# Performance work log

Measured on AMD Instinct MI355X. Metric: run time of the kernel, lower is better.

The kernel has to match this reference:

```python
import jax, jax.numpy as jnp
import numpy as np

N, C, H, W = 4, 256, 64, 64  # in_channels == out_channels == C


def conv1x1(x, w, b):
    # x: [N, Cin, H, W], w: [Cout, Cin], b: [Cout]
    return jnp.einsum('nchw,oc->nohw', x, w) + b[None, :, None, None]


def setup_inputs() -> dict:
    key = jax.random.key(0)
    ks = jax.random.split(key, 4)
    scale = 1.0 / np.sqrt(C)
    return {
        'x': jax.random.normal(ks[0], (N, C, H, W), dtype=jnp.float32),
        'theta_w': jax.random.normal(ks[1], (C, C), dtype=jnp.float32) * scale,
        'theta_b': jnp.zeros((C,), dtype=jnp.float32),
        'phi_w': jax.random.normal(ks[2], (C, C), dtype=jnp.float32) * scale,
        'phi_b': jnp.zeros((C,), dtype=jnp.float32),
        'conv1_w': jax.random.normal(ks[3], (C, C), dtype=jnp.float32) * scale,
        'conv1_b': jnp.zeros((C,), dtype=jnp.float32),
    }


def reference(x, theta_w, theta_b, phi_w, phi_b, conv1_w, conv1_b):
    n, c, h, w = x.shape
    hw = h * w
    theta = conv1x1(x, theta_w, theta_b).reshape(n, c, hw)   # queries [N,C,HW]
    phi = conv1x1(x, phi_w, phi_b).reshape(n, c, hw)         # keys    [N,C,HW]
    g = x.reshape(n, c, hw)                                   # values  [N,C,HW]
    # f = einsum('niab,nicd->nabcd') flattened: [N, HW_q, HW_k]
    scores = jnp.einsum('ncp,ncq->npq', theta, phi) / jnp.sqrt(jnp.asarray(c, x.dtype))
    attn = jax.nn.softmax(scores, axis=-1)                    # softmax over keys
    # f = einsum('nabcd,nicd->niab'): weighted sum of values
    f = jnp.einsum('npq,ncq->ncp', attn, g).reshape(n, c, h, w)
    result = conv1x1(f, conv1_w, conv1_b)
    return x + result
```

## Files before the change

### kernel.cpp

```cpp
#include <hip/hip_runtime.h>
#include <hip/hip_bf16.h>

typedef __attribute__((ext_vector_type(8))) short short8;
typedef __attribute__((ext_vector_type(4))) short short4_t;
typedef __attribute__((ext_vector_type(4))) float float4_t;
typedef unsigned short ushort;

#define HW 4096
#define CC 256
#define NBATCH 4
#define SEQ ((size_t)NBATCH * HW)

static __device__ __forceinline__ unsigned short f2b(float f) {
    union { float f; unsigned u; } v; v.f = f;
    unsigned r = v.u + 0x7FFF + ((v.u >> 16) & 1);
    return (unsigned short)(r >> 16);
}
static __device__ __forceinline__ float b2f(unsigned short u) {
    union { unsigned u; float f; } v; v.u = ((unsigned)u) << 16;
    return v.f;
}

__global__ __launch_bounds__(256) void k_prep(const float* __restrict__ x,
                                              const float* __restrict__ tw,
                                              const float* __restrict__ pw,
                                              const float* __restrict__ cw,
                                              unsigned short* __restrict__ XT,
                                              unsigned short* __restrict__ gb,
                                              unsigned short* __restrict__ Wbt,
                                              unsigned short* __restrict__ Wbp,
                                              unsigned short* __restrict__ Wbc) {
    __shared__ float T[64][65];
    int fb = blockIdx.x + 64 * (blockIdx.y + 4 * blockIdx.z);
    if (fb < 768) {
        int i = fb * 256 + threadIdx.x;
        int sel = i >> 16, off = i & 65535;
        const float* s = sel == 0 ? tw : (sel == 1 ? pw : cw);
        unsigned short* d = sel == 0 ? Wbt : (sel == 1 ? Wbp : Wbc);
        d[off] = f2b(s[off]);
    }
    int n = blockIdx.z, c0 = blockIdx.y * 64, p0 = blockIdx.x * 64;
    int t = threadIdx.x;
    int pl = t & 63, rg = t >> 6;
    const float* xp = x + ((size_t)n * CC + c0) * HW + p0;
    #pragma unroll
    for (int i = 0; i < 16; i++) {
        int cl = rg * 16 + i;
        float v = xp[(size_t)cl * HW + pl];
        T[cl][pl] = v;
        gb[((size_t)n * CC + c0 + cl) * HW + p0 + pl] = f2b(v);
    }
    __syncthreads();
    int cl = t & 63, pg = t >> 6;
    unsigned short* xt = XT + ((size_t)n * HW + p0) * CC + c0;
    #pragma unroll
    for (int i = 0; i < 16; i++) {
        int plw = pg * 16 + i;
        xt[(size_t)plw * CC + cl] = f2b(T[cl][plw]);
    }
}

__global__ __launch_bounds__(256) void k_proj(const unsigned short* __restrict__ XT,
                                              const unsigned short* __restrict__ Wt,
                                              const unsigned short* __restrict__ Wp,
                                              const float* __restrict__ bt,
                                              const float* __restrict__ bp,
                                              unsigned short* __restrict__ outT_t,
                                              unsigned short* __restrict__ outT_p) {
    const unsigned short* W; const float* b; unsigned short* outT;
    if (blockIdx.y == 0) { W = Wt; b = bt; outT = outT_t; }
    else                 { W = Wp; b = bp; outT = outT_p; }
    int w = threadIdx.x >> 6, lane = threadIdx.x & 63;
    int nidx = lane & 15, quad = lane >> 4;
    size_t row0 = (size_t)blockIdx.x * 64 + w * 16;
    float4_t acc[16];
    #pragma unroll
    for (int i = 0; i < 16; i++) acc[i] = (float4_t)(0.f);
    const unsigned short* arow = XT + (row0 + nidx) * CC + quad * 8;
    for (int ks = 0; ks < 8; ks++) {
        short8 a = *(const short8*)(arow + ks * 32);
        #pragma unroll
        for (int cb = 0; cb < 16; cb++) {
            short8 bb = *(const short8*)(W + (size_t)(cb * 16 + nidx) * CC + ks * 32 + quad * 8);
            acc[cb] = __builtin_amdgcn_mfma_f32_16x16x32_bf16(a, bb, acc[cb], 0, 0, 0);
        }
    }
    #pragma unroll
    for (int cb = 0; cb < 16; cb++) {
        int co = cb * 16 + nidx;
        float bias = b[co];
        #pragma unroll
        for (int r = 0; r < 4; r++) {
            size_t prow = row0 + quad * 4 + r;
            outT[prow * CC + co] = f2b(acc[cb][r] + bias);
        }
    }
}

__global__ __launch_bounds__(512)
void k_attn(const unsigned short* __restrict__ thetaT,
            const unsigned short* __restrict__ phiT,
            const unsigned short* __restrict__ gb,
            ushort* __restrict__ Ow, float* __restrict__ lw) {
    __shared__ __align__(16) ushort Kl[2][16384];
    __shared__ __align__(16) ushort Pbuf[2][16][64][8];
    __shared__ float Lbuf[2][128];

    const int tid = threadIdx.x;
    const int w = tid >> 6, lane = tid & 63;
    const int nidx = lane & 15, quad = lane >> 4;
    const int qg = w & 3;
    const int kh = w >> 2;
    const int nb = (blockIdx.x & 7) >> 1;
    const int h  = blockIdx.x & 1;
    const int qtile = blockIdx.x >> 3;
    const int p0 = qtile * 128;
    const size_t seq0 = (size_t)nb * HW;
    const ushort* Kg = phiT + seq0 * CC;
    const ushort* Vg = gb + (size_t)nb * CC * HW;
    const int k00 = h * 2048;

    short8 th[2][8];
    #pragma unroll
    for (int qs = 0; qs < 2; qs++) {
        const ushort* qrow = thetaT + (seq0 + p0 + qg * 32 + qs * 16 + nidx) * CC + quad * 8;
        #pragma unroll
        for (int kb = 0; kb < 8; kb++) th[qs][kb] = *(const short8*)(qrow + kb * 32);
    }

    float4_t o[2][8];
    #pragma unroll
    for (int i = 0; i < 2; i++)
        #pragma unroll
        for (int j = 0; j < 8; j++) o[i][j] = (float4_t)(0.f);
    float lrow[2] = {0.f, 0.f};

    const int c_s = tid >> 4, n_s = tid & 15;
    const int kfbase = (c_s >> 2) * 512 + ((c_s & 3) * 16 + n_s) * 8;
    auto loadKregs = [&](short8 (&kr)[4], int tt) {
        #pragma unroll
        for (int rr = 0; rr < 4; rr++)
            kr[rr] = *(const short8*)(Kg + (size_t)(k00 + tt * 64 + rr * 16 + n_s) * CC + c_s * 8);
    };
    auto stageK = [&](int buf, const short8 (&kr)[4]) {
        #pragma unroll
        for (int rr = 0; rr < 4; rr++) *(short8*)(&Kl[buf][rr * 4096 + kfbase]) = kr[rr];
    };
    auto loadVregs = [&](short8 (&vr)[4], int tt) {
        #pragma unroll
        for (int mg = 0; mg < 2; mg++)
            #pragma unroll
            for (int kst = 0; kst < 2; kst++)
                vr[mg * 2 + kst] = *(const short8*)(Vg + (size_t)(w * 32 + mg * 16 + nidx) * HW
                                                    + k00 + tt * 64 + kst * 32 + quad * 8);
    };

    const float SC = 0.0625f * 1.44269504088896f;
    const int Gp = quad >> 1;
    const int pcell_lo = (nidx ^ (Gp * 4));
    const int pj0 = (quad & 1) * 4;
    const int prcell = ((lane >> 4) << 4) | ((lane & 15) ^ (((lane >> 4) & 1) * 4));

    float4_t s00, s01, s10, s11;
    auto expPhase = [&](int buf) {
        short4_t pk;
        #pragma unroll
        for (int r = 0; r < 4; r++) {
            float e = exp2f(s00[r] * SC); lrow[0] += e; pk[r] = (short)f2b(e);
        }
        *(short4_t*)(&Pbuf[buf][(qg * 2 + 0) * 2 + kh][(0 * 2 + Gp) * 16 + pcell_lo][pj0]) = pk;
        #pragma unroll
        for (int r = 0; r < 4; r++) {
            float e = exp2f(s01[r] * SC); lrow[1] += e; pk[r] = (short)f2b(e);
        }
        *(short4_t*)(&Pbuf[buf][(qg * 2 + 1) * 2 + kh][(0 * 2 + Gp) * 16 + pcell_lo][pj0]) = pk;
        #pragma unroll
        for (int r = 0; r < 4; r++) {
            float e = exp2f(s10[r] * SC); lrow[0] += e; pk[r] = (short)f2b(e);
        }
        *(short4_t*)(&Pbuf[buf][(qg * 2 + 0) * 2 + kh][(1 * 2 + Gp) * 16 + pcell_lo][pj0]) = pk;
        #pragma unroll
        for (int r = 0; r < 4; r++) {
            float e = exp2f(s11[r] * SC); lrow[1] += e; pk[r] = (short)f2b(e);
        }
        *(short4_t*)(&Pbuf[buf][(qg * 2 + 1) * 2 + kh][(1 * 2 + Gp) * 16 + pcell_lo][pj0]) = pk;
    };

    short8 kregs[4], vA[4], vB[4];

    auto ITER = [&](int t, const short8 (&vCur)[4], short8 (&vNext)[4]) {
        const int pb = t & 1;
        const int kbuf = (t + 1) & 1;
        s00 = (float4_t)(0.f); s01 = (float4_t)(0.f);
        s10 = (float4_t)(0.f); s11 = (float4_t)(0.f);
        #pragma unroll
        for (int i = 0; i < 8; i++) {
            short8 k0 = *(const short8*)(&Kl[kbuf][((kh * 2 + 0) * 8 + i) * 512 + lane * 8]);
            short8 k1 = *(const short8*)(&Kl[kbuf][((kh * 2 + 1) * 8 + i) * 512 + lane * 8]);
            s00 = __builtin_amdgcn_mfma_f32_16x16x32_bf16(k0, th[0][i], s00, 0, 0, 0);
            s01 = __builtin_amdgcn_mfma_f32_16x16x32_bf16(k0, th[1][i], s01, 0, 0, 0);
            s10 = __builtin_amdgcn_mfma_f32_16x16x32_bf16(k1, th[0][i], s10, 0, 0, 0);
            s11 = __builtin_amdgcn_mfma_f32_16x16x32_bf16(k1, th[1][i], s11, 0, 0, 0);
            short8 pf0 = *(const short8*)(&Pbuf[pb][i * 2 + 0][prcell][0]);
            short8 pf1 = *(const short8*)(&Pbuf[pb][i * 2 + 1][prcell][0]);
            o[0][i] = __builtin_amdgcn_mfma_f32_16x16x32_bf16(vCur[0], pf0, o[0][i], 0, 0, 0);
            o[0][i] = __builtin_amdgcn_mfma_f32_16x16x32_bf16(vCur[1], pf1, o[0][i], 0, 0, 0);
            o[1][i] = __builtin_amdgcn_mfma_f32_16x16x32_bf16(vCur[2], pf0, o[1][i], 0, 0, 0);
            o[1][i] = __builtin_amdgcn_mfma_f32_16x16x32_bf16(vCur[3], pf1, o[1][i], 0, 0, 0);
        }
        loadVregs(vNext, t + 1);
        expPhase((t + 1) & 1);
        if (t < 30) {
            stageK((t + 2) & 1, kregs);
            loadKregs(kregs, (t + 3 < 32) ? t + 3 : 31);
        }
        __syncthreads();
    };

    loadKregs(kregs, 0); loadVregs(vA, 0);
    stageK(0, kregs);
    loadKregs(kregs, 1);
    __syncthreads();
    s00 = (float4_t)(0.f); s01 = (float4_t)(0.f); s10 = (float4_t)(0.f); s11 = (float4_t)(0.f);
    #pragma unroll
    for (int kb = 0; kb < 8; kb++) {
        short8 k0 = *(const short8*)(&Kl[0][((kh * 2 + 0) * 8 + kb) * 512 + lane * 8]);
        short8 k1 = *(const short8*)(&Kl[0][((kh * 2 + 1) * 8 + kb) * 512 + lane * 8]);
        s00 = __builtin_amdgcn_mfma_f32_16x16x32_bf16(k0, th[0][kb], s00, 0, 0, 0);
        s01 = __builtin_amdgcn_mfma_f32_16x16x32_bf16(k0, th[1][kb], s01, 0, 0, 0);
        s10 = __builtin_amdgcn_mfma_f32_16x16x32_bf16(k1, th[0][kb], s10, 0, 0, 0);
        s11 = __builtin_amdgcn_mfma_f32_16x16x32_bf16(k1, th[1][kb], s11, 0, 0, 0);
    }
    expPhase(0);
    stageK(1, kregs);
    loadKregs(kregs, 2);
    __syncthreads();

    #pragma unroll 1
    for (int tt = 0; tt < 15; tt++) {
        ITER(tt * 2, vA, vB);
        ITER(tt * 2 + 1, vB, vA);
    }
    ITER(30, vA, vB);
    #pragma unroll
    for (int i = 0; i < 8; i++) {
        short8 pf0 = *(const short8*)(&Pbuf[1][i * 2 + 0][prcell][0]);
        short8 pf1 = *(const short8*)(&Pbuf[1][i * 2 + 1][prcell][0]);
        o[0][i] = __builtin_amdgcn_mfma_f32_16x16x32_bf16(vB[0], pf0, o[0][i], 0, 0, 0);
        o[0][i] = __builtin_amdgcn_mfma_f32_16x16x32_bf16(vB[1], pf1, o[0][i], 0, 0, 0);
        o[1][i] = __builtin_amdgcn_mfma_f32_16x16x32_bf16(vB[2], pf0, o[1][i], 0, 0, 0);
        o[1][i] = __builtin_amdgcn_mfma_f32_16x16x32_bf16(vB[3], pf1, o[1][i], 0, 0, 0);
    }

    #pragma unroll
    for (int qs = 0; qs < 2; qs++) {
        float v = lrow[qs];
        v += __shfl_xor(v, 16);
        v += __shfl_xor(v, 32);
        if (quad == 0) Lbuf[kh][qg * 32 + qs * 16 + nidx] = v;
    }
    __syncthreads();
    if (tid < 128)
        lw[(size_t)h * SEQ + seq0 + p0 + tid] = Lbuf[0][tid] + Lbuf[1][tid];
    ushort* Op = Ow + ((size_t)h * SEQ + seq0 + p0) * CC;
    #pragma unroll
    for (int mg = 0; mg < 2; mg++)
        #pragma unroll
        for (int qq = 0; qq < 8; qq++) {
            short4_t pk;
            #pragma unroll
            for (int r = 0; r < 4; r++) pk[r] = (short)f2b(o[mg][qq][r]);
            *(short4_t*)(Op + (size_t)(qq * 16 + nidx) * CC + w * 32 + mg * 16 + quad * 4) = pk;
        }
}

__global__ __launch_bounds__(256) void k_reduce(const ushort* __restrict__ Ow,
                                                const float* __restrict__ lw,
                                                unsigned short* __restrict__ fT) {
    const short8* O0 = (const short8*)Ow;
    const short8* O1 = (const short8*)(Ow + SEQ * CC);
    int i0 = blockIdx.x * 256 + threadIdx.x;
    #pragma unroll
    for (int j = 0; j < 4; j++) {
        int idx = j * 131072 + i0;
        int row = idx >> 5;
        float li = 1.0f / (lw[row] + lw[SEQ + row]);
        short8 a = O0[idx];
        short8 b = O1[idx];
        short8 pk;
        #pragma unroll
        for (int r = 0; r < 8; r++)
            pk[r] = (short)f2b((b2f((ushort)a[r]) + b2f((ushort)b[r])) * li);
        *(short8*)(fT + (size_t)idx * 8) = pk;
    }
}

__global__ __launch_bounds__(256) void k_final(const unsigned short* __restrict__ Wc,
                                               const float* __restrict__ bc,
                                               const unsigned short* __restrict__ fT,
                                               const float* __restrict__ x,
                                               float* __restrict__ out) {
    int w = threadIdx.x >> 6, lane = threadIdx.x & 63;
    int nidx = lane & 15, quad = lane >> 4;
    int n = blockIdx.z;
    int co0 = blockIdx.y * 64 + w * 16;
    int p0 = blockIdx.x * 64;
    float4_t acc[4];
    #pragma unroll
    for (int i = 0; i < 4; i++) acc[i] = (float4_t)(0.f);
    const unsigned short* arow = Wc + (size_t)(co0 + nidx) * CC + quad * 8;
    const unsigned short* brow = fT + ((size_t)n * HW + p0 + nidx) * CC + quad * 8;
    for (int ks = 0; ks < 8; ks++) {
        short8 a = *(const short8*)(arow + ks * 32);
        #pragma unroll
        for (int pb = 0; pb < 4; pb++) {
            short8 bb = *(const short8*)(brow + (size_t)pb * 16 * CC + ks * 32);
            acc[pb] = __builtin_amdgcn_mfma_f32_16x16x32_bf16(a, bb, acc[pb], 0, 0, 0);
        }
    }
    #pragma unroll
    for (int pb = 0; pb < 4; pb++) {
        #pragma unroll
        for (int r = 0; r < 4; r++) {
            int co = co0 + quad * 4 + r;
            size_t idx = ((size_t)n * CC + co) * HW + p0 + pb * 16 + nidx;
            out[idx] = x[idx] + bc[co] + acc[pb][r];
        }
    }
}

extern "C" void kernel_launch(void* const* d_in, const int* in_sizes, int n_in,
                              void* d_out, int out_size, void* d_ws, size_t ws_size,
                              hipStream_t stream) {
    const float* x       = (const float*)d_in[0];
    const float* theta_w = (const float*)d_in[1];
    const float* theta_b = (const float*)d_in[2];
    const float* phi_w   = (const float*)d_in[3];
    const float* phi_b   = (const float*)d_in[4];
    const float* conv1_w = (const float*)d_in[5];
    const float* conv1_b = (const float*)d_in[6];
    float* out = (float*)d_out;

    unsigned short* XT  = (unsigned short*)d_ws;
    unsigned short* gb  = XT  + SEQ * CC;
    unsigned short* thT = gb  + SEQ * CC;
    unsigned short* phT = thT + SEQ * CC;
    unsigned short* fT  = phT + SEQ * CC;
    unsigned short* Wbt = fT  + SEQ * CC;
    unsigned short* Wbp = Wbt + 65536;
    unsigned short* Wbc = Wbp + 65536;
    unsigned short* Ow  = Wbc + 65536;
    float* lw = (float*)(Ow + 2 * SEQ * CC);

    k_prep<<<dim3(64, 4, 4), 256, 0, stream>>>(x, theta_w, phi_w, conv1_w, XT, gb, Wbt, Wbp, Wbc);
    k_proj<<<dim3(256, 2), 256, 0, stream>>>(XT, Wbt, Wbp, theta_b, phi_b, thT, phT);
    k_attn<<<dim3(256), 512, 0, stream>>>(thT, phT, gb, Ow, lw);
    k_reduce<<<dim3(512), 256, 0, stream>>>(Ow, lw, fT);
    k_final<<<dim3(64, 4, 4), 256, 0, stream>>>(Wbc, conv1_b, fT, x, out);
}
```

Baseline: 213.4 us.

## Restructure attention kernel into smaller blocks with direct global-to-LDS K staging

The attention kernel now uses 256-thread blocks covering 64 queries each, with 512 blocks instead of 256. It uses a 32-key tile and 64 iterations, and each wave splits the channel dimension of V instead of the key dimension. K tiles are staged with global_load_lds (direct global-to-LDS), which removes the register round-trip and the K prefetch registers. The goal is more resident blocks, lower register and LDS pressure, and fewer staging instructions. The cost is twice as many loop iterations and barriers, and each block re-reads K and V for fewer queries, which doubles global K/V traffic.

Measured after the change: 322.0 us. +50.9%, slower.

```diff
diff --git a/kernel.cpp b/kernel.cpp
--- a/kernel.cpp
+++ b/kernel.cpp
@@ -10,6 +10,12 @@
 #define CC 256
 #define NBATCH 4
 #define SEQ ((size_t)NBATCH * HW)
+#define KT 32
+#define NT 64
+
+#define GLDS(g, l) __builtin_amdgcn_global_load_lds( \
+    (const __attribute__((address_space(1))) void*)(g), \
+    (__attribute__((address_space(3))) void*)(l), 16, 0, 0)
 
 static __device__ __forceinline__ unsigned short f2b(float f) {
     union { float f; unsigned u; } v; v.f = f;
@@ -97,24 +103,24 @@
     }
 }
 
-__global__ __launch_bounds__(512)
+__global__ __launch_bounds__(256)
 void k_attn(const unsigned short* __restrict__ thetaT,
             const unsigned short* __restrict__ phiT,
             const unsigned short* __restrict__ gb,
             ushort* __restrict__ Ow, float* __restrict__ lw) {
-    __shared__ __align__(16) ushort Kl[2][16384];
-    __shared__ __align__(16) ushort Pbuf[2][16][64][8];
-    __shared__ float Lbuf[2][128];
+    __shared__ __align__(16) ushort Kl[2][8192];
+    __shared__ __align__(16) ushort Pbuf[2][4][64][8];
+    __shared__ float Lbuf[2][64];
 
     const int tid = threadIdx.x;
     const int w = tid >> 6, lane = tid & 63;
     const int nidx = lane & 15, quad = lane >> 4;
-    const int qg = w & 3;
-    const int kh = w >> 2;
+    const int qg = w >> 1;
+    const int sub = w & 1;
     const int nb = (blockIdx.x & 7) >> 1;
     const int h  = blockIdx.x & 1;
     const int qtile = blockIdx.x >> 3;
-    const int p0 = qtile * 128;
+    const int p0 = qtile * 64;
     const size_t seq0 = (size_t)nb * HW;
     const ushort* Kg = phiT + seq0 * CC;
     const ushort* Vg = gb + (size_t)nb * CC * HW;
@@ -128,128 +134,91 @@
         for (int kb = 0; kb < 8; kb++) th[qs][kb] = *(const short8*)(qrow + kb * 32);
     }
 
-    float4_t o[2][8];
-    #pragma unroll
-    for (int i = 0; i < 2; i++)
-        #pragma unroll
-        for (int j = 0; j < 8; j++) o[i][j] = (float4_t)(0.f);
+    float4_t o[8][2];
+    #pragma unroll
+    for (int i = 0; i < 8; i++)
+        #pragma unroll
+        for (int j = 0; j < 2; j++) o[i][j] = (float4_t)(0.f);
     float lrow[2] = {0.f, 0.f};
 
-    const int c_s = tid >> 4, n_s = tid & 15;
-    const int kfbase = (c_s >> 2) * 512 + ((c_s & 3) * 16 + n_s) * 8;
-    auto loadKregs = [&](short8 (&kr)[4], int tt) {
-        #pragma unroll
-        for (int rr = 0; rr < 4; rr++)
-            kr[rr] = *(const short8*)(Kg + (size_t)(k00 + tt * 64 + rr * 16 + n_s) * CC + c_s * 8);
+    auto stageK = [&](int buf, int t) {
+        #pragma unroll
+        for (int i = 0; i < 4; i++) {
+            const int f = w * 4 + i;
+            const ushort* gp = Kg + (size_t)(k00 + t * KT + (f >> 3) * 16 + nidx) * CC
+                               + (f & 7) * 32 + quad * 8;
+            GLDS(gp, &Kl[buf][f * 512]);
+        }
     };
-    auto stageK = [&](int buf, const short8 (&kr)[4]) {
-        #pragma unroll
-        for (int rr = 0; rr < 4; rr++) *(short8*)(&Kl[buf][rr * 4096 + kfbase]) = kr[rr];
+    auto loadVregs = [&](short8 (&vr)[8], int t) {
+        #pragma unroll
+        for (int mg = 0; mg < 8; mg++)
+            vr[mg] = *(const short8*)(Vg + (size_t)(sub * 128 + mg * 16 + nidx) * HW
+                                      + k00 + t * KT + quad * 8);
     };
-    auto loadVregs = [&](short8 (&vr)[4], int tt) {
-        #pragma unroll
-        for (int mg = 0; mg < 2; mg++)
-            #pragma unroll
-            for (int kst = 0; kst < 2; kst++)
-                vr[mg * 2 + kst] = *(const short8*)(Vg + (size_t)(w * 32 + mg * 16 + nidx) * HW
-                                                    + k00 + tt * 64 + kst * 32 + quad * 8);
-    };
 
     const float SC = 0.0625f * 1.44269504088896f;
-    const int Gp = quad >> 1;
-    const int pcell_lo = (nidx ^ (Gp * 4));
+    const int pcell = (sub * 2 + (quad >> 1)) * 16 + nidx;
     const int pj0 = (quad & 1) * 4;
-    const int prcell = ((lane >> 4) << 4) | ((lane & 15) ^ (((lane >> 4) & 1) * 4));
-
-    float4_t s00, s01, s10, s11;
+
+    float4_t s0, s1;
     auto expPhase = [&](int buf) {
         short4_t pk;
         #pragma unroll
         for (int r = 0; r < 4; r++) {
-            float e = exp2f(s00[r] * SC); lrow[0] += e; pk[r] = (short)f2b(e);
-        }
-        *(short4_t*)(&Pbuf[buf][(qg * 2 + 0) * 2 + kh][(0 * 2 + Gp) * 16 + pcell_lo][pj0]) = pk;
+            float e = exp2f(s0[r] * SC); lrow[0] += e; pk[r] = (short)f2b(e);
+        }
+        *(short4_t*)(&Pbuf[buf][qg * 2 + 0][pcell][pj0]) = pk;
         #pragma unroll
         for (int r = 0; r < 4; r++) {
-            float e = exp2f(s01[r] * SC); lrow[1] += e; pk[r] = (short)f2b(e);
-        }
-        *(short4_t*)(&Pbuf[buf][(qg * 2 + 1) * 2 + kh][(0 * 2 + Gp) * 16 + pcell_lo][pj0]) = pk;
-        #pragma unroll
-        for (int r = 0; r < 4; r++) {
-            float e = exp2f(s10[r] * SC); lrow[0] += e; pk[r] = (short)f2b(e);
-        }
-        *(short4_t*)(&Pbuf[buf][(qg * 2 + 0) * 2 + kh][(1 * 2 + Gp) * 16 + pcell_lo][pj0]) = pk;
-        #pragma unroll
-        for (int r = 0; r < 4; r++) {
-            float e = exp2f(s11[r] * SC); lrow[1] += e; pk[r] = (short)f2b(e);
-        }
-        *(short4_t*)(&Pbuf[buf][(qg * 2 + 1) * 2 + kh][(1 * 2 + Gp) * 16 + pcell_lo][pj0]) = pk;
+            float e = exp2f(s1[r] * SC); lrow[1] += e; pk[r] = (short)f2b(e);
+        }
+        *(short4_t*)(&Pbuf[buf][qg * 2 + 1][pcell][pj0]) = pk;
     };
 
-    short8 kregs[4], vA[4], vB[4];
-
-    auto ITER = [&](int t, const short8 (&vCur)[4], short8 (&vNext)[4]) {
+    short8 vr[8];
+    stageK(0, 0);
+    __syncthreads();
+    s0 = (float4_t)(0.f); s1 = (float4_t)(0.f);
+    #pragma unroll
+    for (int kb = 0; kb < 8; kb++) {
+        short8 kf = *(const short8*)(&Kl[0][(sub * 8 + kb) * 512 + lane * 8]);
+        s0 = __builtin_amdgcn_mfma_f32_16x16x32_bf16(kf, th[0][kb], s0, 0, 0, 0);
+        s1 = __builtin_amdgcn_mfma_f32_16x16x32_bf16(kf, th[1][kb], s1, 0, 0, 0);
+    }
+    expPhase(0);
+    stageK(1, 1);
+    loadVregs(vr, 0);
+    __syncthreads();
+
+    #pragma unroll 1
+    for (int t = 0; t < NT - 1; t++) {
         const int pb = t & 1;
         const int kbuf = (t + 1) & 1;
-        s00 = (float4_t)(0.f); s01 = (float4_t)(0.f);
-        s10 = (float4_t)(0.f); s11 = (float4_t)(0.f);
+        short8 pf0 = *(const short8*)(&Pbuf[pb][qg * 2 + 0][lane][0]);
+        short8 pf1 = *(const short8*)(&Pbuf[pb][qg * 2 + 1][lane][0]);
+        s0 = (float4_t)(0.f); s1 = (float4_t)(0.f);
         #pragma unroll
         for (int i = 0; i < 8; i++) {
-            short8 k0 = *(const short8*)(&Kl[kbuf][((kh * 2 + 0) * 8 + i) * 512 + lane * 8]);
-            short8 k1 = *(const short8*)(&Kl[kbuf][((kh * 2 + 1) * 8 + i) * 512 + lane * 8]);
-            s00 = __builtin_amdgcn_mfma_f32_16x16x32_bf16(k0, th[0][i], s00, 0, 0, 0);
-            s01 = __builtin_amdgcn_mfma_f32_16x16x32_bf16(k0, th[1][i], s01, 0, 0, 0);
-            s10 = __builtin_amdgcn_mfma_f32_16x16x32_bf16(k1, th[0][i], s10, 0, 0, 0);
-            s11 = __builtin_amdgcn_mfma_f32_16x16x32_bf16(k1, th[1][i], s11, 0, 0, 0);
-            short8 pf0 = *(const short8*)(&Pbuf[pb][i * 2 + 0][prcell][0]);
-            short8 pf1 = *(const short8*)(&Pbuf[pb][i * 2 + 1][prcell][0]);
-            o[0][i] = __builtin_amdgcn_mfma_f32_16x16x32_bf16(vCur[0], pf0, o[0][i], 0, 0, 0);
-            o[0][i] = __builtin_amdgcn_mfma_f32_16x16x32_bf16(vCur[1], pf1, o[0][i], 0, 0, 0);
-            o[1][i] = __builtin_amdgcn_mfma_f32_16x16x32_bf16(vCur[2], pf0, o[1][i], 0, 0, 0);
-            o[1][i] = __builtin_amdgcn_mfma_f32_16x16x32_bf16(vCur[3], pf1, o[1][i], 0, 0, 0);
-        }
-        loadVregs(vNext, t + 1);
+            short8 kf = *(const short8*)(&Kl[kbuf][(sub * 8 + i) * 512 + lane * 8]);
+            s0 = __builtin_amdgcn_mfma_f32_16x16x32_bf16(kf, th[0][i], s0, 0, 0, 0);
+            s1 = __builtin_amdgcn_mfma_f32_16x16x32_bf16(kf, th[1][i], s1, 0, 0, 0);
+            o[i][0] = __builtin_amdgcn_mfma_f32_16x16x32_bf16(vr[i], pf0, o[i][0], 0, 0, 0);
+            o[i][1] = __builtin_amdgcn_mfma_f32_16x16x32_bf16(vr[i], pf1, o[i][1], 0, 0, 0);
+        }
+        loadVregs(vr, t + 1);
         expPhase((t + 1) & 1);
-        if (t < 30) {
-            stageK((t + 2) & 1, kregs);
-            loadKregs(kregs, (t + 3 < 32) ? t + 3 : 31);
-        }
+        if (t < NT - 2) stageK(t & 1, t + 2);
         __syncthreads();
-    };
-
-    loadKregs(kregs, 0); loadVregs(vA, 0);
-    stageK(0, kregs);
-    loadKregs(kregs, 1);
-    __syncthreads();
-    s00 = (float4_t)(0.f); s01 = (float4_t)(0.f); s10 = (float4_t)(0.f); s11 = (float4_t)(0.f);
-    #pragma unroll
-    for (int kb = 0; kb < 8; kb++) {
-        short8 k0 = *(const short8*)(&Kl[0][((kh * 2 + 0) * 8 + kb) * 512 + lane * 8]);
-        short8 k1 = *(const short8*)(&Kl[0][((kh * 2 + 1) * 8 + kb) * 512 + lane * 8]);
-        s00 = __builtin_amdgcn_mfma_f32_16x16x32_bf16(k0, th[0][kb], s00, 0, 0, 0);
-        s01 = __builtin_amdgcn_mfma_f32_16x16x32_bf16(k0, th[1][kb], s01, 0, 0, 0);
-        s10 = __builtin_amdgcn_mfma_f32_16x16x32_bf16(k1, th[0][kb], s10, 0, 0, 0);
-        s11 = __builtin_amdgcn_mfma_f32_16x16x32_bf16(k1, th[1][kb], s11, 0, 0, 0);
-    }
-    expPhase(0);
-    stageK(1, kregs);
-    loadKregs(kregs, 2);
-    __syncthreads();
-
-    #pragma unroll 1
-    for (int tt = 0; tt < 15; tt++) {
-        ITER(tt * 2, vA, vB);
-        ITER(tt * 2 + 1, vB, vA);
-    }
-    ITER(30, vA, vB);
-    #pragma unroll
-    for (int i = 0; i < 8; i++) {
-        short8 pf0 = *(const short8*)(&Pbuf[1][i * 2 + 0][prcell][0]);
-        short8 pf1 = *(const short8*)(&Pbuf[1][i * 2 + 1][prcell][0]);
-        o[0][i] = __builtin_amdgcn_mfma_f32_16x16x32_bf16(vB[0], pf0, o[0][i], 0, 0, 0);
-        o[0][i] = __builtin_amdgcn_mfma_f32_16x16x32_bf16(vB[1], pf1, o[0][i], 0, 0, 0);
-        o[1][i] = __builtin_amdgcn_mfma_f32_16x16x32_bf16(vB[2], pf0, o[1][i], 0, 0, 0);
-        o[1][i] = __builtin_amdgcn_mfma_f32_16x16x32_bf16(vB[3], pf1, o[1][i], 0, 0, 0);
+    }
+    {
+        short8 pf0 = *(const short8*)(&Pbuf[(NT - 1) & 1][qg * 2 + 0][lane][0]);
+        short8 pf1 = *(const short8*)(&Pbuf[(NT - 1) & 1][qg * 2 + 1][lane][0]);
+        #pragma unroll
+        for (int i = 0; i < 8; i++) {
+            o[i][0] = __builtin_amdgcn_mfma_f32_16x16x32_bf16(vr[i], pf0, o[i][0], 0, 0, 0);
+            o[i][1] = __builtin_amdgcn_mfma_f32_16x16x32_bf16(vr[i], pf1, o[i][1], 0, 0, 0);
+        }
     }
 
     #pragma unroll
@@ -257,20 +226,21 @@
         float v = lrow[qs];
         v += __shfl_xor(v, 16);
         v += __shfl_xor(v, 32);
-        if (quad == 0) Lbuf[kh][qg * 32 + qs * 16 + nidx] = v;
+        if (quad == 0) Lbuf[sub][qg * 32 + qs * 16 + nidx] = v;
     }
     __syncthreads();
-    if (tid < 128)
+    if (tid < 64)
         lw[(size_t)h * SEQ + seq0 + p0 + tid] = Lbuf[0][tid] + Lbuf[1][tid];
     ushort* Op = Ow + ((size_t)h * SEQ + seq0 + p0) * CC;
     #pragma unroll
-    for (int mg = 0; mg < 2; mg++)
-        #pragma unroll
-        for (int qq = 0; qq < 8; qq++) {
+    for (int mg = 0; mg < 8; mg++)
+        #pragma unroll
+        for (int qt2 = 0; qt2 < 2; qt2++) {
             short4_t pk;
             #pragma unroll
-            for (int r = 0; r < 4; r++) pk[r] = (short)f2b(o[mg][qq][r]);
-            *(short4_t*)(Op + (size_t)(qq * 16 + nidx) * CC + w * 32 + mg * 16 + quad * 4) = pk;
+            for (int r = 0; r < 4; r++) pk[r] = (short)f2b(o[mg][qt2][r]);
+            *(short4_t*)(Op + (size_t)(qg * 32 + qt2 * 16 + nidx) * CC
+                         + sub * 128 + mg * 16 + quad * 4) = pk;
         }
 }
 
@@ -354,7 +324,7 @@
 
     k_prep<<<dim3(64, 4, 4), 256, 0, stream>>>(x, theta_w, phi_w, conv1_w, XT, gb, Wbt, Wbp, Wbc);
     k_proj<<<dim3(256, 2), 256, 0, stream>>>(XT, Wbt, Wbp, theta_b, phi_b, thT, phT);
-    k_attn<<<dim3(256), 512, 0, stream>>>(thT, phT, gb, Ow, lw);
+    k_attn<<<dim3(512), 256, 0, stream>>>(thT, phT, gb, Ow, lw);
     k_reduce<<<dim3(512), 256, 0, stream>>>(Ow, lw, fT);
     k_final<<<dim3(64, 4, 4), 256, 0, stream>>>(Wbc, conv1_b, fT, x, out);
 }
```
